# Optimization experiments

Measured on AMD Instinct MI355X. Metric: run time of the kernel, lower is better.

Reference implementation:

```python
import jax, jax.numpy as jnp
import numpy as np

IN_CH = 2
K = 5
STRIDE = 1
NQ = IN_CH * K          # n_qubits = kernel_size * in_channels
DIM = 2 ** NQ           # quantum state dimension = 1024


def setup_inputs() -> dict:
    key = jax.random.key(0)
    k1, k2, k3 = jax.random.split(key, 3)
    x = jax.random.normal(k1, (16, IN_CH, 4096), dtype=jnp.float32)
    entangle_matrix = jax.random.normal(k2, (DIM, DIM), dtype=jnp.float32) / np.sqrt(DIM).astype(np.float32)
    theta = jax.random.uniform(k3, (NQ,), dtype=jnp.float32, minval=0.0, maxval=2.0 * np.pi)
    return {"x": x, "entangle_matrix": entangle_matrix, "theta": theta}


def _im2col(x):
    # torch: unfold(-1,K,stride) -> (B,C,nW,K); cat over channel dim along -1 -> (B,nW,C*K)
    B, C, L = x.shape
    nW = (L - K) // STRIDE + 1
    idx = jnp.arange(nW)[:, None] * STRIDE + jnp.arange(K)[None, :]   # (nW, K)
    cols = x[:, :, idx]                                               # (B, C, nW, K)
    cols = jnp.transpose(cols, (0, 2, 1, 3)).reshape(B * nW, C * K)   # channel-major last dim
    return cols, nW


def reference(x, entangle_matrix, theta):
    cols, nW = _im2col(x)           # (N, NQ) rotation angles, one per qubit
    N = cols.shape[0]
    # --- RY(x_i) angle encoding from |0...0>: product state of [cos(x/2), sin(x/2)] ---
    half = 0.5 * cols
    c, s = jnp.cos(half), jnp.sin(half)          # (N, NQ)
    state = jnp.ones((N, 1), dtype=x.dtype)
    for i in range(NQ):                          # loop over fixed small n_qubits
        qi = jnp.stack([c[:, i], s[:, i]], axis=-1)            # (N, 2)
        state = (state[:, :, None] * qi[:, None, :]).reshape(N, -1)
    # --- entangling layer: psi' = E @ psi (the custom kernel matmul) ---
    state = state @ entangle_matrix.T            # (N, DIM)
    # --- trainable per-qubit RY(theta_i) layer ---
    ct, st = jnp.cos(0.5 * theta), jnp.sin(0.5 * theta)
    for i in range(NQ):
        s4 = state.reshape(N, 2 ** i, 2, 2 ** (NQ - 1 - i))
        a0, a1 = s4[:, :, 0], s4[:, :, 1]
        state = jnp.stack([ct[i] * a0 - st[i] * a1,
                           st[i] * a0 + ct[i] * a1], axis=2).reshape(N, DIM)
    # --- measure <Z> on qubit 0 (most significant bit) ---
    p = (state * state).reshape(N, 2, DIM // 2)
    z = p[:, 0].sum(-1) - p[:, 1].sum(-1)        # (N,)
    B = x.shape[0]
    return z.reshape(B, 1, -1, nW)
```

## Files before the change

kernel.cpp:

```cpp
#include <hip/hip_runtime.h>
#include <math.h>

#define B_SZ   16
#define L_SZ   4096
#define NWIN   4092
#define U3     243
#define UPAD   256

#define APK_OFF 0
#define M_OFF   65536
#define EXTRA_OFF (M_OFF + 1048576)

typedef __attribute__((ext_vector_type(8))) __bf16 bf16x8;
typedef __attribute__((ext_vector_type(4))) float f32x4;

__device__ __forceinline__ float sel3(int t, float c, float s) {
    return t == 0 ? 1.0f : (t == 1 ? c : s);
}

__device__ __forceinline__ int apk_idx(int u, int v) {
    return (((u >> 4) * 8 + (v >> 5)) * 64 + ((u & 15) | (((v >> 3) & 3) << 4))) * 8 + (v & 7);
}

__device__ __forceinline__ void bfsplit(float x, float& hf, float& lf) {
    hf = __uint_as_float(__float_as_uint(x) & 0xFFFF0000u);
    lf = x - hf;
}

__global__ __launch_bounds__(256, 4) void mgemm_ker(const float* __restrict__ E,
                                                    const float* __restrict__ theta,
                                                    float* __restrict__ M,
                                                    float* __restrict__ Mp_extra) {
    __shared__ float SA[32][72];
    __shared__ float SB[32][72];
    __shared__ uint4 AfH[4 * 64], AfL[4 * 64];
    __shared__ uint4 BfH[4 * 64], BfL[4 * 64];

    int t = blockIdx.x;
    int bj = 0;
    while (t >= 16 - bj) { t -= 16 - bj; ++bj; }
    int bk = bj + t;
    int ks = blockIdx.z;
    int tid = threadIdx.x;
    int lane = tid & 63;
    int wave = tid >> 6;

    float th = theta[0];
    float st, ct;
    __sincosf(th, &st, &ct);

    f32x4 acc[4];
    #pragma unroll
    for (int kt = 0; kt < 4; ++kt) acc[kt] = (f32x4){0.f, 0.f, 0.f, 0.f};

    int kchunk = 1024 / gridDim.z;
    int k0 = ks * kchunk;
    int lr = tid >> 3;
    int lcq = (tid & 7) * 8;

    for (int d0 = k0; d0 < k0 + kchunk; d0 += 32) {
        bool hi = d0 >= 512;
        int dp = hi ? (d0 - 512) : (d0 + 512);
        float4 a0 = *(const float4*)&E[(d0 + lr) * 1024 + bj * 64 + lcq];
        float4 a1 = *(const float4*)&E[(d0 + lr) * 1024 + bj * 64 + lcq + 4];
        float4 q0 = *(const float4*)&E[(d0 + lr) * 1024 + bk * 64 + lcq];
        float4 q1 = *(const float4*)&E[(d0 + lr) * 1024 + bk * 64 + lcq + 4];
        float4 p0 = *(const float4*)&E[(dp + lr) * 1024 + bk * 64 + lcq];
        float4 p1 = *(const float4*)&E[(dp + lr) * 1024 + bk * 64 + lcq + 4];
        float4 y0, y1;
        if (!hi) {
            y0.x = ct * q0.x - st * p0.x; y0.y = ct * q0.y - st * p0.y;
            y0.z = ct * q0.z - st * p0.z; y0.w = ct * q0.w - st * p0.w;
            y1.x = ct * q1.x - st * p1.x; y1.y = ct * q1.y - st * p1.y;
            y1.z = ct * q1.z - st * p1.z; y1.w = ct * q1.w - st * p1.w;
        } else {
            y0.x = -st * p0.x - ct * q0.x; y0.y = -st * p0.y - ct * q0.y;
            y0.z = -st * p0.z - ct * q0.z; y0.w = -st * p0.w - ct * q0.w;
            y1.x = -st * p1.x - ct * q1.x; y1.y = -st * p1.y - ct * q1.y;
            y1.z = -st * p1.z - ct * q1.z; y1.w = -st * p1.w - ct * q1.w;
        }
        __syncthreads();
        *(float4*)&SA[lr][lcq] = a0;
        *(float4*)&SA[lr][lcq + 4] = a1;
        *(float4*)&SB[lr][lcq] = y0;
        *(float4*)&SB[lr][lcq + 4] = y1;
        __syncthreads();

        {
            unsigned ahw[4], alw[4], bhw[4], blw[4];
            float pah, pal, pbh, pbl;
            #pragma unroll
            for (int i = 0; i < 8; ++i) {
                float av = SA[wave * 8 + i][lane];
                float bv = SB[wave * 8 + i][lane];
                float ah, al, bh, bl;
                bfsplit(av, ah, al);
                bfsplit(bv, bh, bl);
                if (i & 1) {
                    ahw[i >> 1] = __byte_perm(__float_as_uint(pah), __float_as_uint(ah), 0x7632);
                    alw[i >> 1] = __byte_perm(__float_as_uint(pal), __float_as_uint(al), 0x7632);
                    bhw[i >> 1] = __byte_perm(__float_as_uint(pbh), __float_as_uint(bh), 0x7632);
                    blw[i >> 1] = __byte_perm(__float_as_uint(pbl), __float_as_uint(bl), 0x7632);
                } else { pah = ah; pal = al; pbh = bh; pbl = bl; }
            }
            int slot = ((lane >> 4) << 6) + (lane & 15) + (wave << 4);
            AfH[slot] = make_uint4(ahw[0], ahw[1], ahw[2], ahw[3]);
            AfL[slot] = make_uint4(alw[0], alw[1], alw[2], alw[3]);
            BfH[slot] = make_uint4(bhw[0], bhw[1], bhw[2], bhw[3]);
            BfL[slot] = make_uint4(blw[0], blw[1], blw[2], blw[3]);
        }
        __syncthreads();

        uint4 ahu = AfH[wave * 64 + lane];
        uint4 alu = AfL[wave * 64 + lane];
        bf16x8 ah = __builtin_bit_cast(bf16x8, ahu);
        bf16x8 al = __builtin_bit_cast(bf16x8, alu);
        #pragma unroll
        for (int kt = 0; kt < 4; ++kt) {
            uint4 bhu = BfH[kt * 64 + lane];
            uint4 blu = BfL[kt * 64 + lane];
            bf16x8 bh = __builtin_bit_cast(bf16x8, bhu);
            bf16x8 bl = __builtin_bit_cast(bf16x8, blu);
            acc[kt] = __builtin_amdgcn_mfma_f32_16x16x32_bf16(ah, bh, acc[kt], 0, 0, 0);
            acc[kt] = __builtin_amdgcn_mfma_f32_16x16x32_bf16(ah, bl, acc[kt], 0, 0, 0);
            acc[kt] = __builtin_amdgcn_mfma_f32_16x16x32_bf16(al, bh, acc[kt], 0, 0, 0);
        }
    }

    float* dst = (ks == 0) ? M : (Mp_extra + (ks - 1) * 1048576);
    #pragma unroll
    for (int kt = 0; kt < 4; ++kt) {
        #pragma unroll
        for (int i = 0; i < 4; ++i) {
            int r = bj * 64 + wave * 16 + ((lane >> 4) << 2) + i;
            int c = bk * 64 + kt * 16 + (lane & 15);
            dst[((r >> 5) * 32 + (c >> 5)) * 1024 + (r & 31) * 32 + (c & 31)] = acc[kt][i];
        }
    }
}

__global__ __launch_bounds__(256) void sum_ker(float* __restrict__ M,
                                               const float* __restrict__ Mp_extra,
                                               int S) {
    int i = blockIdx.x * 256 + threadIdx.x;
    float4 v = ((const float4*)M)[i];
    for (int s = 1; s < S; ++s) {
        float4 p = ((const float4*)(Mp_extra + (s - 1) * 1048576))[i];
        v.x += p.x; v.y += p.y; v.z += p.z; v.w += p.w;
    }
    ((float4*)M)[i] = v;
}

__global__ __launch_bounds__(256) void cwht_ker(const float* __restrict__ M,
                                                unsigned short* __restrict__ ApkH) {
    __shared__ float D[1024];
    int mx = blockIdx.x;
    int mxh = mx >> 5, mxl = mx & 31;
    int tid = threadIdx.x;
    float v[4];
    #pragma unroll
    for (int k = 0; k < 4; ++k) {
        int j = tid + k * 256;
        int jh = j >> 5, jl = j & 31;
        int kh = jh ^ mxh, kl = jl ^ mxl;
        int off;
        if ((jh >> 1) <= (kh >> 1)) off = ((jh * 32 + kh) * 32 + jl) * 32 + kl;
        else                        off = ((kh * 32 + jh) * 32 + kl) * 32 + jl;
        v[k] = M[off];
    }
    #pragma unroll
    for (int s = 0; s < 6; ++s) {
        int bit = (tid >> s) & 1;
        #pragma unroll
        for (int k = 0; k < 4; ++k) {
            float p = __shfl_xor(v[k], 1 << s, 64);
            v[k] = bit ? (p - v[k]) : (v[k] + p);
        }
    }
    #pragma unroll
    for (int k = 0; k < 4; ++k) D[tid + k * 256] = v[k];
    __syncthreads();
    {
        int b6 = (tid >> 6) & 1, b7 = (tid >> 7) & 1;
        #pragma unroll
        for (int k = 0; k < 4; ++k) {
            float p64  = D[(tid ^ 64)  + k * 256];
            float p128 = D[(tid ^ 128) + k * 256];
            float p192 = D[(tid ^ 192) + k * 256];
            float ta = b6 ? (p64 - v[k])   : (v[k] + p64);
            float tb = b6 ? (p192 - p128)  : (p128 + p192);
            v[k] = b7 ? (tb - ta) : (ta + tb);
        }
    }
    {
        float a0 = v[0] + v[1], a1 = v[0] - v[1], a2 = v[2] + v[3], a3 = v[2] - v[3];
        v[0] = a0 + a2; v[1] = a1 + a3; v[2] = a0 - a2; v[3] = a1 - a3;
    }
    #pragma unroll
    for (int k = 0; k < 4; ++k) {
        int mz = tid + k * 256;
        if (mz & mx) continue;
        int u = 0, vv = 0;
        #pragma unroll
        for (int i = 0; i < 5; ++i) {
            int bit = 9 - i;
            int tt = ((mx >> bit) & 1) ? 2 : (((mz >> bit) & 1) ? 1 : 0);
            u = u * 3 + tt;
        }
        #pragma unroll
        for (int i = 5; i < 10; ++i) {
            int bit = 9 - i;
            int tt = ((mx >> bit) & 1) ? 2 : (((mz >> bit) & 1) ? 1 : 0);
            vv = vv * 3 + tt;
        }
        float val = v[k] * (1.0f / 1024.0f);
        unsigned hh = __float_as_uint(val) & 0xFFFF0000u;
        float lf = val - __uint_as_float(hh);
        unsigned ll = __float_as_uint(lf) >> 16;
        int idx = apk_idx(u, vv);
        ApkH[idx] = (unsigned short)(hh >> 16);
        ApkH[idx + 65536] = (unsigned short)ll;
    }
    if (mx == 0) {
        for (int e = tid; e < 13 * 256; e += 256) {
            int u = 243 + (e >> 8), vv = e & 255;
            int idx = apk_idx(u, vv);
            ApkH[idx] = 0; ApkH[idx + 65536] = 0;
        }
        for (int e = tid; e < 243 * 13; e += 256) {
            int u = e / 13, vv = 243 + (e - (e / 13) * 13);
            int idx = apk_idx(u, vv);
            ApkH[idx] = 0; ApkH[idx + 65536] = 0;
        }
    }
}

__global__ __launch_bounds__(256, 2) void main_ker(const float* __restrict__ x,
                                                   const uint4* __restrict__ Apk,
                                                   float* __restrict__ out) {
    __shared__ float trg[4][68];
    __shared__ __align__(16) unsigned char arena[33280];
    unsigned short* F1h = (unsigned short*)arena;
    unsigned short* F1l = (unsigned short*)(arena + 16640);
    float* F0 = (float*)arena;
    __shared__ float red[16][16];

    int tid = threadIdx.x;
    int w0 = blockIdx.x * 64;
    int b  = blockIdx.y;
    int lane = tid & 63;
    int wave = tid >> 6;
    int wb = tid & 63;
    int wu = __builtin_amdgcn_readfirstlane(wave);

    for (int p = tid; p < 68; p += 256) {
        int pos = w0 + p;
        bool ok = pos < L_SZ;
        float x1 = ok ? x[b * 8192 + 4096 + pos] : 0.f;
        float x0 = ok ? x[b * 8192 + pos] : 0.f;
        float c1v, s1v, c0v, s0v;
        __sincosf(x1, &s1v, &c1v);
        __sincosf(x0, &s0v, &c0v);
        if (!ok) { c1v = 0.f; s1v = 0.f; c0v = 0.f; s0v = 0.f; }
        trg[0][p] = c1v; trg[1][p] = s1v; trg[2][p] = c0v; trg[3][p] = s0v;
    }

    f32x4 acc[4][4];
    #pragma unroll
    for (int ut = 0; ut < 4; ++ut)
        #pragma unroll
        for (int wt = 0; wt < 4; ++wt)
            acc[ut][wt] = (f32x4){0.f, 0.f, 0.f, 0.f};

    __syncthreads();

    float c1r[5], s1r[5];
    #pragma unroll
    for (int k = 0; k < 5; ++k) { c1r[k] = trg[0][wb + k]; s1r[k] = trg[1][wb + k]; }

    const uint4* Ahi = Apk;
    const uint4* Alo = Apk + 8192;

    uint4 a_h[4], a_l[4];
    #pragma unroll
    for (int ut = 0; ut < 4; ++ut) {
        int idx = ((wave * 4 + ut) * 8 + 0) * 64 + lane;
        a_h[ut] = Ahi[idx];
        a_l[ut] = Alo[idx];
    }

    #pragma unroll 1
    for (int h = 0; h < 2; ++h) {
        if (h) __syncthreads();
        {
            int gv = h * 128 + wu * 32;
            int t0 = gv / 81; int rr = gv - t0 * 81;
            int t1 = rr / 27; rr -= t1 * 27;
            int t2 = rr / 9;  rr -= t2 * 9;
            int t3 = rr / 3;  int t4 = rr - t3 * 3;
            float g0 = sel3(t0, c1r[0], s1r[0]);
            float g1 = sel3(t1, c1r[1], s1r[1]);
            float g2 = sel3(t2, c1r[2], s1r[2]);
            float g3 = sel3(t3, c1r[3], s1r[3]);
            float p0123 = g0 * g1 * g2 * g3;
            #pragma unroll
            for (int p8 = 0; p8 < 4; ++p8) {
                unsigned hw[4], lw[4];
                float prevh, prevl;
                #pragma unroll
                for (int i = 0; i < 8; ++i) {
                    float val = p0123 * sel3(t4, c1r[4], s1r[4]);
                    float hf, lf;
                    bfsplit(val, hf, lf);
                    if (i & 1) {
                        hw[i >> 1] = __byte_perm(__float_as_uint(prevh), __float_as_uint(hf), 0x7632);
                        lw[i >> 1] = __byte_perm(__float_as_uint(prevl), __float_as_uint(lf), 0x7632);
                    } else { prevh = hf; prevl = lf; }
                    if (++t4 == 3) { t4 = 0;
                        if (++t3 == 3) { t3 = 0;
                            if (++t2 == 3) { t2 = 0;
                                if (++t1 == 3) { t1 = 0; ++t0; g0 = sel3(t0, c1r[0], s1r[0]); }
                                g1 = sel3(t1, c1r[1], s1r[1]);
                            }
                            g2 = sel3(t2, c1r[2], s1r[2]);
                        }
                        g3 = sel3(t3, c1r[3], s1r[3]);
                        p0123 = g0 * g1 * g2 * g3;
                    }
                }
                int vp = wu * 4 + p8;
                *(uint4*)&F1h[(vp * 65 + wb) * 8] = make_uint4(hw[0], hw[1], hw[2], hw[3]);
                *(uint4*)&F1l[(vp * 65 + wb) * 8] = make_uint4(lw[0], lw[1], lw[2], lw[3]);
            }
        }
        __syncthreads();

        #pragma unroll
        for (int kl = 0; kl < 4; ++kl) {
            int ks = h * 4 + kl;
            uint4 na_h[4], na_l[4];
            if (ks < 7) {
                #pragma unroll
                for (int ut = 0; ut < 4; ++ut) {
                    int idx = ((wave * 4 + ut) * 8 + ks + 1) * 64 + lane;
                    na_h[ut] = Ahi[idx];
                    na_l[ut] = Alo[idx];
                }
            }
            int vp = kl * 4 + (lane >> 4);
            #pragma unroll
            for (int wt = 0; wt < 4; ++wt) {
                int off = (vp * 65 + wt * 16 + (lane & 15)) * 8;
                uint4 b_h = *(const uint4*)&F1h[off];
                uint4 b_l = *(const uint4*)&F1l[off];
                bf16x8 bh = __builtin_bit_cast(bf16x8, b_h);
                bf16x8 bl = __builtin_bit_cast(bf16x8, b_l);
                #pragma unroll
                for (int ut = 0; ut < 4; ++ut) {
                    bf16x8 ah = __builtin_bit_cast(bf16x8, a_h[ut]);
                    bf16x8 al = __builtin_bit_cast(bf16x8, a_l[ut]);
                    acc[ut][wt] = __builtin_amdgcn_mfma_f32_16x16x32_bf16(ah, bh, acc[ut][wt], 0, 0, 0);
                    acc[ut][wt] = __builtin_amdgcn_mfma_f32_16x16x32_bf16(ah, bl, acc[ut][wt], 0, 0, 0);
                    acc[ut][wt] = __builtin_amdgcn_mfma_f32_16x16x32_bf16(al, bh, acc[ut][wt], 0, 0, 0);
                }
            }
            if (ks < 7) {
                #pragma unroll
                for (int ut = 0; ut < 4; ++ut) { a_h[ut] = na_h[ut]; a_l[ut] = na_l[ut]; }
            }
        }
    }

    int c = lane & 15;
    float c0b[5], s0b[5];
    #pragma unroll
    for (int k = 0; k < 5; ++k) { c0b[k] = trg[2][wb + k]; s0b[k] = trg[3][wb + k]; }
    float zcol[4] = {0.f, 0.f, 0.f, 0.f};

    __syncthreads();
    #pragma unroll 1
    for (int hp = 0; hp < 2; ++hp) {
        if (hp) __syncthreads();
        {
            int gu = hp * 128 + wu * 32;
            int t0 = gu / 81; int rr = gu - t0 * 81;
            int t1 = rr / 27; rr -= t1 * 27;
            int t2 = rr / 9;  rr -= t2 * 9;
            int t3 = rr / 3;  int t4 = rr - t3 * 3;
            float g0 = sel3(t0, c0b[0], s0b[0]);
            float g1 = sel3(t1, c0b[1], s0b[1]);
            float g2 = sel3(t2, c0b[2], s0b[2]);
            float g3 = sel3(t3, c0b[3], s0b[3]);
            float p0123 = g0 * g1 * g2 * g3;
            #pragma unroll
            for (int s = 0; s < 32; ++s) {
                float val = p0123 * sel3(t4, c0b[4], s0b[4]);
                F0[(wu * 32 + s) * 65 + wb] = val;
                if (++t4 == 3) { t4 = 0;
                    if (++t3 == 3) { t3 = 0;
                        if (++t2 == 3) { t2 = 0;
                            if (++t1 == 3) { t1 = 0; ++t0; g0 = sel3(t0, c0b[0], s0b[0]); }
                            g1 = sel3(t1, c0b[1], s0b[1]);
                        }
                        g2 = sel3(t2, c0b[2], s0b[2]);
                    }
                    g3 = sel3(t3, c0b[3], s0b[3]);
                    p0123 = g0 * g1 * g2 * g3;
                }
            }
        }
        __syncthreads();
        if ((wave >> 1) == hp) {
            int wloc = wave & 1;
            int qb = (lane >> 4) << 2;
            #pragma unroll
            for (int ut = 0; ut < 4; ++ut) {
                #pragma unroll
                for (int r = 0; r < 4; ++r) {
                    int uloc = wloc * 64 + ut * 16 + qb + r;
                    #pragma unroll
                    for (int wt = 0; wt < 4; ++wt)
                        zcol[wt] += F0[uloc * 65 + wt * 16 + c] * acc[ut][wt][r];
                }
            }
        }
    }

    #pragma unroll
    for (int wt = 0; wt < 4; ++wt) {
        float v = zcol[wt];
        v += __shfl_xor(v, 16, 64);
        v += __shfl_xor(v, 32, 64);
        if ((lane >> 4) == 0) red[wave * 4 + wt][lane] = v;
    }
    __syncthreads();
    if (tid < 64) {
        int wt = tid >> 4, cc = tid & 15;
        float z = red[0 * 4 + wt][cc] + red[1 * 4 + wt][cc]
                + red[2 * 4 + wt][cc] + red[3 * 4 + wt][cc];
        int w = wt * 16 + cc;
        if (w0 + w < NWIN) out[b * NWIN + w0 + w] = z;
    }
}

extern "C" void kernel_launch(void* const* d_in, const int* in_sizes, int n_in,
                              void* d_out, int out_size, void* d_ws, size_t ws_size,
                              hipStream_t stream) {
    const float* x     = (const float*)d_in[0];
    const float* E     = (const float*)d_in[1];
    const float* theta = (const float*)d_in[2];
    float* out = (float*)d_out;
    float* ws = (float*)d_ws;

    uint4* Apk = (uint4*)(ws + APK_OFF);
    float* M   = ws + M_OFF;
    float* Mx  = ws + EXTRA_OFF;

    size_t need4 = (size_t)(EXTRA_OFF + 3 * 1048576) * 4;
    size_t need2 = (size_t)(EXTRA_OFF + 1 * 1048576) * 4;
    int S = (ws_size >= need4) ? 4 : ((ws_size >= need2) ? 2 : 1);

    mgemm_ker<<<dim3(136, 1, S), 256, 0, stream>>>(E, theta, M, Mx);
    if (S > 1) sum_ker<<<1024, 256, 0, stream>>>(M, Mx, S);
    cwht_ker<<<1024, 256, 0, stream>>>(M, (unsigned short*)Apk);
    main_ker<<<dim3(64, 16), 256, 0, stream>>>(x, Apk, out);
}
```

Before: 70.62 us.

## Drop low-bf16 split of encoded state in first GEMM, raise occupancy

```diff
diff --git a/kernel.cpp b/kernel.cpp
--- a/kernel.cpp
+++ b/kernel.cpp
@@ -235,13 +235,12 @@
     }
 }
 
-__global__ __launch_bounds__(256, 2) void main_ker(const float* __restrict__ x,
+__global__ __launch_bounds__(256, 3) void main_ker(const float* __restrict__ x,
                                                    const uint4* __restrict__ Apk,
                                                    float* __restrict__ out) {
     __shared__ float trg[4][68];
     __shared__ __align__(16) unsigned char arena[33280];
     unsigned short* F1h = (unsigned short*)arena;
-    unsigned short* F1l = (unsigned short*)(arena + 16640);
     float* F0 = (float*)arena;
     __shared__ float red[16][16];
 
@@ -280,14 +279,6 @@
 
     const uint4* Ahi = Apk;
     const uint4* Alo = Apk + 8192;
-
-    uint4 a_h[4], a_l[4];
-    #pragma unroll
-    for (int ut = 0; ut < 4; ++ut) {
-        int idx = ((wave * 4 + ut) * 8 + 0) * 64 + lane;
-        a_h[ut] = Ahi[idx];
-        a_l[ut] = Alo[idx];
-    }
 
     #pragma unroll 1
     for (int h = 0; h < 2; ++h) {
@@ -305,17 +296,14 @@
             float p0123 = g0 * g1 * g2 * g3;
             #pragma unroll
             for (int p8 = 0; p8 < 4; ++p8) {
-                unsigned hw[4], lw[4];
-                float prevh, prevl;
+                unsigned hw[4];
+                unsigned prevr;
                 #pragma unroll
                 for (int i = 0; i < 8; ++i) {
                     float val = p0123 * sel3(t4, c1r[4], s1r[4]);
-                    float hf, lf;
-                    bfsplit(val, hf, lf);
-                    if (i & 1) {
-                        hw[i >> 1] = __byte_perm(__float_as_uint(prevh), __float_as_uint(hf), 0x7632);
-                        lw[i >> 1] = __byte_perm(__float_as_uint(prevl), __float_as_uint(lf), 0x7632);
-                    } else { prevh = hf; prevl = lf; }
+                    unsigned rb = (__float_as_uint(val) + 0x8000u) >> 16;
+                    if (i & 1) hw[i >> 1] = prevr | (rb << 16);
+                    else       prevr = rb;
                     if (++t4 == 3) { t4 = 0;
                         if (++t3 == 3) { t3 = 0;
                             if (++t2 == 3) { t2 = 0;
@@ -330,7 +318,6 @@
                 }
                 int vp = wu * 4 + p8;
                 *(uint4*)&F1h[(vp * 65 + wb) * 8] = make_uint4(hw[0], hw[1], hw[2], hw[3]);
-                *(uint4*)&F1l[(vp * 65 + wb) * 8] = make_uint4(lw[0], lw[1], lw[2], lw[3]);
             }
         }
         __syncthreads();
@@ -338,35 +325,26 @@
         #pragma unroll
         for (int kl = 0; kl < 4; ++kl) {
             int ks = h * 4 + kl;
-            uint4 na_h[4], na_l[4];
-            if (ks < 7) {
-                #pragma unroll
-                for (int ut = 0; ut < 4; ++ut) {
-                    int idx = ((wave * 4 + ut) * 8 + ks + 1) * 64 + lane;
-                    na_h[ut] = Ahi[idx];
-                    na_l[ut] = Alo[idx];
-                }
+            uint4 a_h[4], a_l[4];
+            #pragma unroll
+            for (int ut = 0; ut < 4; ++ut) {
+                int idx = ((wave * 4 + ut) * 8 + ks) * 64 + lane;
+                a_h[ut] = Ahi[idx];
+                a_l[ut] = Alo[idx];
             }
             int vp = kl * 4 + (lane >> 4);
             #pragma unroll
             for (int wt = 0; wt < 4; ++wt) {
                 int off = (vp * 65 + wt * 16 + (lane & 15)) * 8;
-                uint4 b_h = *(const uint4*)&F1h[off];
-                uint4 b_l = *(const uint4*)&F1l[off];
-                bf16x8 bh = __builtin_bit_cast(bf16x8, b_h);
-                bf16x8 bl = __builtin_bit_cast(bf16x8, b_l);
+                uint4 b_u = *(const uint4*)&F1h[off];
+                bf16x8 bb = __builtin_bit_cast(bf16x8, b_u);
                 #pragma unroll
                 for (int ut = 0; ut < 4; ++ut) {
                     bf16x8 ah = __builtin_bit_cast(bf16x8, a_h[ut]);
                     bf16x8 al = __builtin_bit_cast(bf16x8, a_l[ut]);
-                    acc[ut][wt] = __builtin_amdgcn_mfma_f32_16x16x32_bf16(ah, bh, acc[ut][wt], 0, 0, 0);
-                    acc[ut][wt] = __builtin_amdgcn_mfma_f32_16x16x32_bf16(ah, bl, acc[ut][wt], 0, 0, 0);
-                    acc[ut][wt] = __builtin_amdgcn_mfma_f32_16x16x32_bf16(al, bh, acc[ut][wt], 0, 0, 0);
+                    acc[ut][wt] = __builtin_amdgcn_mfma_f32_16x16x32_bf16(ah, bb, acc[ut][wt], 0, 0, 0);
+                    acc[ut][wt] = __builtin_amdgcn_mfma_f32_16x16x32_bf16(al, bb, acc[ut][wt], 0, 0, 0);
                 }
-            }
-            if (ks < 7) {
-                #pragma unroll
-                for (int ut = 0; ut < 4; ++ut) { a_h[ut] = na_h[ut]; a_l[ut] = na_l[ut]; }
             }
         }
     }
```

Measured after the change: 67.58 us. -4.3%, faster.
